# Performance work log

Hardware: AMD Instinct MI355X
Metric: run time of the kernel (lower is better)

## Reference

```python
import jax, jax.numpy as jnp
import numpy as np
from jax import lax

B, LATENT, SEQ, HID, OUT = 4096, 128, 512, 32, 64


def setup_inputs() -> dict:
    key = jax.random.key(0)
    ks = jax.random.split(key, 9)
    s = 1.0 / np.sqrt(HID)  # PyTorch-style init scale
    f32 = jnp.float32
    return {
        "z": jax.random.normal(ks[0], (B, LATENT), f32),
        "init_W": jax.random.uniform(ks[1], (HID, LATENT), f32, -s, s),
        "init_b": jax.random.uniform(ks[2], (HID,), f32, -s, s),
        "W_ih": jax.random.uniform(ks[3], (4 * HID, HID), f32, -s, s),
        "W_hh": jax.random.uniform(ks[4], (4 * HID, HID), f32, -s, s),
        "b_ih": jax.random.uniform(ks[5], (4 * HID,), f32, -s, s),
        "b_hh": jax.random.uniform(ks[6], (4 * HID,), f32, -s, s),
        "out_W": jax.random.uniform(ks[7], (OUT, HID), f32, -s, s),
        "out_b": jax.random.uniform(ks[8], (OUT,), f32, -s, s),
    }


def reference(z, init_W, init_b, W_ih, W_hh, b_ih, b_hh, out_W, out_b):
    # init_fc: z -> h0 (num_layers=1); cell starts at zero
    h0 = z @ init_W.T + init_b  # [B, H]
    c0 = jnp.zeros_like(h0)

    # x_in is all zeros, so the input-to-hidden term is a constant bias;
    # compute it once (keeps W_ih in the graph, matmul with zeros == 0).
    x_zero = jnp.zeros((z.shape[0], W_ih.shape[1]), z.dtype)
    gate_const = x_zero @ W_ih.T + b_ih + b_hh  # [B, 4H]

    def step(carry, _):
        h, c = carry
        gates = h @ W_hh.T + gate_const  # [B, 4H], PyTorch gate order i,f,g,o
        i, f, g, o = jnp.split(gates, 4, axis=-1)
        i = jax.nn.sigmoid(i)
        f = jax.nn.sigmoid(f)
        g = jnp.tanh(g)
        o = jax.nn.sigmoid(o)
        c = f * c + i * g
        h = o * jnp.tanh(c)
        return (h, c), h

    _, hs = lax.scan(step, (h0, c0), None, length=SEQ)  # [T, B, H]
    out = jnp.transpose(hs, (1, 0, 2))  # [B, T, H] (batch_first)
    y = out @ out_W.T + out_b  # [B, T, OUT]
    return y
```

## Files before the change

### kernel.cpp

```cpp
#include <hip/hip_runtime.h>


#define B_SZ   4096
#define LATENT 128
#define SEQ    512
#define HID    32
#define OUT_N  64
#define ROWS   16
#define LSW    40

typedef _Float16 f16x8 __attribute__((ext_vector_type(8)));
typedef _Float16 f16x4 __attribute__((ext_vector_type(4)));
typedef float    f32x4 __attribute__((ext_vector_type(4)));

__device__ __forceinline__ float fexp2(float x) { return __builtin_amdgcn_exp2f(x); }
__device__ __forceinline__ float frcp(float x)  { return __builtin_amdgcn_rcpf(x); }
__device__ __forceinline__ float sigm(float x) {
    return frcp(1.f + fexp2(-1.44269504088896341f * x));
}
__device__ __forceinline__ float tanh_f(float x) {
    return fmaf(-2.f, frcp(1.f + fexp2(2.88539008177792681f * x)), 1.f);
}
__device__ __forceinline__ void lds_barrier() {
    asm volatile("s_waitcnt lgkmcnt(0)\n\ts_barrier" ::: "memory");
}

__global__ __launch_bounds__(512)
void lstm_tr8(const float* __restrict__ z,
              const float* __restrict__ init_W,
              const float* __restrict__ init_b,
              const float* __restrict__ W_hh,
              const float* __restrict__ b_ih,
              const float* __restrict__ b_hh,
              const float* __restrict__ out_W,
              const float* __restrict__ out_b,
              float* __restrict__ y)
{
    __shared__ __align__(16) _Float16 hst[ROWS * LSW];
    __shared__ __align__(8) unsigned short hx[2][2][64][4];

    const int tid  = threadIdx.x;
    const int w    = tid >> 6;
    const int lane = tid & 63;
    const int n_   = lane & 15;
    const int kb   = lane >> 4;
    const int jj   = w & 1;
    const int r_   = w >> 1;
    const int rbase = blockIdx.x * ROWS;

    f16x8 wf[4];
    f32x4 bacc[4];
#pragma unroll
    for (int m = 0; m < 4; m++) {
        int g = 2 * m + jj;
        const float* row = W_hh + (size_t)(16 * g + n_) * HID;
        f16x8 v;
#pragma unroll
        for (int rr = 0; rr < 4; rr++) {
            v[rr]     = (_Float16)row[4 * kb + rr];
            v[4 + rr] = (_Float16)row[4 * kb + 16 + rr];
        }
        wf[m] = v;
        f32x4 b;
#pragma unroll
        for (int r = 0; r < 4; r++) {
            int G = 16 * g + 4 * kb + r;
            b[r] = b_ih[G] + b_hh[G];
        }
        bacc[m] = b;
    }
    f16x8 owf;
    f32x4 oacc;
    {
        int p = r_;
        const float* row = out_W + (size_t)(16 * p + n_) * HID;
        f16x8 v;
#pragma unroll
        for (int rr = 0; rr < 4; rr++) {
            v[rr]     = (_Float16)row[4 * kb + rr];
            v[4 + rr] = (_Float16)row[4 * kb + 16 + rr];
        }
        owf = v;
#pragma unroll
        for (int r = 0; r < 4; r++) oacc[r] = out_b[16 * p + 4 * kb + r];
    }

    {
        int m = tid >> 5, j = tid & 31;
        const float4* zp = (const float4*)(z + (size_t)(rbase + m) * LATENT);
        const float4* wp = (const float4*)(init_W + (size_t)j * LATENT);
        float acc = init_b[j];
#pragma unroll
        for (int k = 0; k < LATENT / 4; k++) {
            float4 a4 = zp[k], b4 = wp[k];
            acc = fmaf(a4.x, b4.x, acc); acc = fmaf(a4.y, b4.y, acc);
            acc = fmaf(a4.z, b4.z, acc); acc = fmaf(a4.w, b4.w, acc);
        }
        hst[m * LSW + j] = (_Float16)acc;
    }
    __syncthreads();

    f16x8 a;
    {
        f16x4 lo = *(const f16x4*)&hst[n_ * LSW + 4 * kb];
        f16x4 hi = *(const f16x4*)&hst[n_ * LSW + 4 * kb + 16];
#pragma unroll
        for (int r = 0; r < 4; r++) { a[r] = lo[r]; a[4 + r] = hi[r]; }
    }

    float c1 = 0.f;

    float* yb = y + (size_t)(rbase + n_) * SEQ * OUT_N + 16 * r_ + 4 * kb;

    for (int t = 0; t < SEQ; t += 4) {
#pragma unroll
        for (int u = 0; u < 4; u++) {
            const int par = u & 1;
            f32x4 acc[4];
#pragma unroll
            for (int m = 0; m < 4; m++)
                acc[m] = __builtin_amdgcn_mfma_f32_16x16x32_f16(wf[m], a, bacc[m], 0, 0, 0);

            {
                float gi = sigm(acc[0][r_]);
                float gf = sigm(acc[1][r_]);
                float gg = tanh_f(acc[2][r_]);
                float go = sigm(acc[3][r_]);
                float cn = fmaf(gf, c1, gi * gg);
                c1 = cn;
                union { _Float16 h; unsigned short u16; } cv;
                cv.h = (_Float16)(go * tanh_f(cn));
                hx[par][jj][lane][r_] = cv.u16;
            }
            lds_barrier();

            f16x4 lo = *(const f16x4*)&hx[par][0][lane][0];
            f16x4 hi = *(const f16x4*)&hx[par][1][lane][0];
#pragma unroll
            for (int r = 0; r < 4; r++) { a[r] = lo[r]; a[4 + r] = hi[r]; }

            if (jj == 0) {
                f32x4 py = __builtin_amdgcn_mfma_f32_16x16x32_f16(owf, a, oacc, 0, 0, 0);
                *(f32x4*)(yb + (size_t)(t + u) * OUT_N) = py;
            }
        }
    }
}

extern "C" void kernel_launch(void* const* d_in, const int* in_sizes, int n_in,
                              void* d_out, int out_size, void* d_ws, size_t ws_size,
                              hipStream_t stream) {
    const float* z      = (const float*)d_in[0];
    const float* init_W = (const float*)d_in[1];
    const float* init_b = (const float*)d_in[2];
    const float* W_hh   = (const float*)d_in[4];
    const float* b_ih   = (const float*)d_in[5];
    const float* b_hh   = (const float*)d_in[6];
    const float* out_W  = (const float*)d_in[7];
    const float* out_b  = (const float*)d_in[8];
    float* yout = (float*)d_out;

    lstm_tr8<<<B_SZ / ROWS, 512, 0, stream>>>(z, init_W, init_b, W_hh, b_ih, b_hh,
                                              out_W, out_b, yout);
}
```

Before: 635.3 us.

## Split output projection onto dedicated consumer waves in a 768-thread block

Adds four producer-consumer waves that do only the output-projection MFMA and global store, so the eight recurrent waves no longer carry that work on the critical serial path. The h exchange buffer grows from double to quad buffering, indexed by the unrolled step. The gate MFMAs and activations are also reordered so the forget/input/cell update starts before the output gate. In exchange the block is larger, which may reduce occupancy, and all twelve waves still meet at the per-step barrier.

```diff
diff --git a/kernel.cpp b/kernel.cpp
--- a/kernel.cpp
+++ b/kernel.cpp
@@ -25,67 +25,69 @@
     asm volatile("s_waitcnt lgkmcnt(0)\n\ts_barrier" ::: "memory");
 }
 
-__global__ __launch_bounds__(512)
-void lstm_tr8(const float* __restrict__ z,
-              const float* __restrict__ init_W,
-              const float* __restrict__ init_b,
-              const float* __restrict__ W_hh,
-              const float* __restrict__ b_ih,
-              const float* __restrict__ b_hh,
-              const float* __restrict__ out_W,
-              const float* __restrict__ out_b,
-              float* __restrict__ y)
+__global__ __launch_bounds__(768)
+void lstm_pc(const float* __restrict__ z,
+             const float* __restrict__ init_W,
+             const float* __restrict__ init_b,
+             const float* __restrict__ W_hh,
+             const float* __restrict__ b_ih,
+             const float* __restrict__ b_hh,
+             const float* __restrict__ out_W,
+             const float* __restrict__ out_b,
+             float* __restrict__ y)
 {
     __shared__ __align__(16) _Float16 hst[ROWS * LSW];
-    __shared__ __align__(8) unsigned short hx[2][2][64][4];
+    __shared__ __align__(8) unsigned short hx[4][2][64][4];
 
     const int tid  = threadIdx.x;
     const int w    = tid >> 6;
     const int lane = tid & 63;
     const int n_   = lane & 15;
     const int kb   = lane >> 4;
+    const bool rec = (w < 8);
     const int jj   = w & 1;
-    const int r_   = w >> 1;
+    const int r_   = (w >> 1) & 3;
+    const int p_   = w - 8;
     const int rbase = blockIdx.x * ROWS;
 
     f16x8 wf[4];
     f32x4 bacc[4];
+    if (rec) {
 #pragma unroll
-    for (int m = 0; m < 4; m++) {
-        int g = 2 * m + jj;
-        const float* row = W_hh + (size_t)(16 * g + n_) * HID;
+        for (int m = 0; m < 4; m++) {
+            int g = 2 * m + jj;
+            const float* row = W_hh + (size_t)(16 * g + n_) * HID;
+            f16x8 v;
+#pragma unroll
+            for (int rr = 0; rr < 4; rr++) {
+                v[rr]     = (_Float16)row[4 * kb + rr];
+                v[4 + rr] = (_Float16)row[4 * kb + 16 + rr];
+            }
+            wf[m] = v;
+            f32x4 b;
+#pragma unroll
+            for (int r = 0; r < 4; r++) {
+                int G = 16 * g + 4 * kb + r;
+                b[r] = b_ih[G] + b_hh[G];
+            }
+            bacc[m] = b;
+        }
+    } else {
+        const float* row = out_W + (size_t)(16 * p_ + n_) * HID;
         f16x8 v;
 #pragma unroll
         for (int rr = 0; rr < 4; rr++) {
             v[rr]     = (_Float16)row[4 * kb + rr];
             v[4 + rr] = (_Float16)row[4 * kb + 16 + rr];
         }
-        wf[m] = v;
+        wf[0] = v;
         f32x4 b;
 #pragma unroll
-        for (int r = 0; r < 4; r++) {
-            int G = 16 * g + 4 * kb + r;
-            b[r] = b_ih[G] + b_hh[G];
-        }
-        bacc[m] = b;
-    }
-    f16x8 owf;
-    f32x4 oacc;
-    {
-        int p = r_;
-        const float* row = out_W + (size_t)(16 * p + n_) * HID;
-        f16x8 v;
-#pragma unroll
-        for (int rr = 0; rr < 4; rr++) {
-            v[rr]     = (_Float16)row[4 * kb + rr];
-            v[4 + rr] = (_Float16)row[4 * kb + 16 + rr];
-        }
-        owf = v;
-#pragma unroll
-        for (int r = 0; r < 4; r++) oacc[r] = out_b[16 * p + 4 * kb + r];
+        for (int r = 0; r < 4; r++) b[r] = out_b[16 * p_ + 4 * kb + r];
+        bacc[0] = b;
     }
 
-    {
+    if (tid < 512) {
         int m = tid >> 5, j = tid & 31;
         const float4* zp = (const float4*)(z + (size_t)(rbase + m) * LATENT);
         const float4* wp = (const float4*)(init_W + (size_t)j * LATENT);
@@ -101,7 +103,7 @@
     __syncthreads();
 
     f16x8 a;
-    {
+    if (rec) {
         f16x4 lo = *(const f16x4*)&hst[n_ * LSW + 4 * kb];
         f16x4 hi = *(const f16x4*)&hst[n_ * LSW + 4 * kb + 16];
 #pragma unroll
@@ -110,37 +112,37 @@
 
     float c1 = 0.f;
 
-    float* yb = y + (size_t)(rbase + n_) * SEQ * OUT_N + 16 * r_ + 4 * kb;
+    float* yb = y + (size_t)(rbase + n_) * SEQ * OUT_N + 16 * p_ + 4 * kb;
 
     for (int t = 0; t < SEQ; t += 4) {
 #pragma unroll
         for (int u = 0; u < 4; u++) {
-            const int par = u & 1;
-            f32x4 acc[4];
-#pragma unroll
-            for (int m = 0; m < 4; m++)
-                acc[m] = __builtin_amdgcn_mfma_f32_16x16x32_f16(wf[m], a, bacc[m], 0, 0, 0);
-
-            {
-                float gi = sigm(acc[0][r_]);
-                float gf = sigm(acc[1][r_]);
-                float gg = tanh_f(acc[2][r_]);
-                float go = sigm(acc[3][r_]);
+            if (rec) {
+                f32x4 af = __builtin_amdgcn_mfma_f32_16x16x32_f16(wf[1], a, bacc[1], 0, 0, 0);
+                f32x4 ai = __builtin_amdgcn_mfma_f32_16x16x32_f16(wf[0], a, bacc[0], 0, 0, 0);
+                f32x4 ag = __builtin_amdgcn_mfma_f32_16x16x32_f16(wf[2], a, bacc[2], 0, 0, 0);
+                f32x4 ao = __builtin_amdgcn_mfma_f32_16x16x32_f16(wf[3], a, bacc[3], 0, 0, 0);
+                float gf = sigm(af[r_]);
+                float gi = sigm(ai[r_]);
+                float gg = tanh_f(ag[r_]);
                 float cn = fmaf(gf, c1, gi * gg);
                 c1 = cn;
+                float go = sigm(ao[r_]);
                 union { _Float16 h; unsigned short u16; } cv;
                 cv.h = (_Float16)(go * tanh_f(cn));
-                hx[par][jj][lane][r_] = cv.u16;
+                hx[u][jj][lane][r_] = cv.u16;
             }
             lds_barrier();
-
-            f16x4 lo = *(const f16x4*)&hx[par][0][lane][0];
-            f16x4 hi = *(const f16x4*)&hx[par][1][lane][0];
+            f16x4 lo = *(const f16x4*)&hx[u][0][lane][0];
+            f16x4 hi = *(const f16x4*)&hx[u][1][lane][0];
+            if (rec) {
 #pragma unroll
-            for (int r = 0; r < 4; r++) { a[r] = lo[r]; a[4 + r] = hi[r]; }
-
-            if (jj == 0) {
-                f32x4 py = __builtin_amdgcn_mfma_f32_16x16x32_f16(owf, a, oacc, 0, 0, 0);
+                for (int r = 0; r < 4; r++) { a[r] = lo[r]; a[4 + r] = hi[r]; }
+            } else {
+                f16x8 ap;
+#pragma unroll
+                for (int r = 0; r < 4; r++) { ap[r] = lo[r]; ap[4 + r] = hi[r]; }
+                f32x4 py = __builtin_amdgcn_mfma_f32_16x16x32_f16(wf[0], ap, bacc[0], 0, 0, 0);
                 *(f32x4*)(yb + (size_t)(t + u) * OUT_N) = py;
             }
         }
@@ -160,6 +162,6 @@
     const float* out_b  = (const float*)d_in[8];
     float* yout = (float*)d_out;
 
-    lstm_tr8<<<B_SZ / ROWS, 512, 0, stream>>>(z, init_W, init_b, W_hh, b_ih, b_hh,
-                                              out_W, out_b, yout);
+    lstm_pc<<<B_SZ / ROWS, 768, 0, stream>>>(z, init_W, init_b, W_hh, b_ih, b_hh,
+                                             out_W, out_b, yout);
 }
```

Measured after the change: 657.2 us. 3.4% more time.
